# Kernel tuning notes

Measured on AMD Instinct MI355X. Metric: run time of the kernel, lower is better.

Reference implementation:

```python
import jax, jax.numpy as jnp
import numpy as np

NB_CLASSES = 100000
SZ_EMBED = 64
SZ_BATCH = 1024


def setup_inputs() -> dict:
    key = jax.random.key(0)
    k1, k2, k3 = jax.random.split(key, 3)
    xs = jax.random.normal(k1, (SZ_BATCH, SZ_EMBED), dtype=jnp.float32)
    ys = jax.random.randint(k2, (SZ_BATCH,), 0, NB_CLASSES, dtype=jnp.int64)
    # xavier_uniform for an Embedding(nb_classes, sz_embed)
    limit = float(np.sqrt(6.0 / (NB_CLASSES + SZ_EMBED)))
    proxies = jax.random.uniform(k3, (NB_CLASSES, SZ_EMBED), dtype=jnp.float32,
                                 minval=-limit, maxval=limit)
    return {"xs": xs, "ys": ys, "proxies": proxies}


def reference(xs, ys, proxies):
    # L2-normalize each proxy row (torch F.normalize; eps guard like torch's 1e-12).
    # Note: the original normalizes the positive proxy with dim=0 on a 1-D vector,
    # which is identical to per-row normalization.
    norms = jnp.linalg.norm(proxies, axis=1, keepdims=True)
    P = proxies / jnp.maximum(norms, 1e-12)                      # [C, D]

    # Squared euclidean distance matrix D[i, c] = ||x_i - P_c||^2 via GEMM
    x_sq = jnp.sum(xs * xs, axis=1, keepdims=True)               # [B, 1]
    p_sq = jnp.sum(P * P, axis=1)                                # [C]
    dist = jnp.maximum(x_sq + p_sq[None, :] - 2.0 * (xs @ P.T), 0.0)  # [B, C]

    logits = -dist                                               # [B, C]
    ys = ys.astype(jnp.int32)
    d_pos = jnp.take_along_axis(dist, ys[:, None], axis=1)[:, 0]  # [B]

    # log sum over negatives (c != y) of exp(-dist)
    neg_mask = jnp.arange(NB_CLASSES)[None, :] != ys[:, None]    # [B, C]
    neg_logits = jnp.where(neg_mask, logits, -jnp.inf)
    log_n = jax.nn.logsumexp(neg_logits, axis=1)                 # [B]

    # -log(p / n) = dist_pos + log(sum_neg exp(-dist))
    per_sample = d_pos + log_n
    return jnp.mean(per_sample)
```

## Files before the change

### kernel.cpp

```cpp
#include <hip/hip_runtime.h>
#include <math.h>

#define B 1024
#define C 100000
#define D 64
#define MT 128
#define TC 256
#define NCH 391
#define NPADROWS (NCH * TC)
#define CPAD (NPADROWS - C)
#define L2E 1.4426950408889634f
#define SCL2 (2.0f * L2E)

typedef __attribute__((ext_vector_type(8))) short short8;
typedef __attribute__((ext_vector_type(4))) float f32x4;

#define WS_PART 0
#define WS_CW2  ((size_t)NCH * B * 4)
#define WS_XBF  (WS_CW2 + B * 4)
#define WS_PBF  (WS_XBF + (size_t)B * D * 2)

#define GLB(p) ((const __attribute__((address_space(1))) void*)(p))
#define LDS(p) ((__attribute__((address_space(3))) void*)(p))

static __device__ __forceinline__ unsigned short f2bf(float f) {
    unsigned u = __float_as_uint(f);
    return (unsigned short)((u + 0x7fffu + ((u >> 16) & 1u)) >> 16);
}
static __device__ __forceinline__ float bf_round(float f) {
    return __uint_as_float(((unsigned)f2bf(f)) << 16);
}
static __device__ __forceinline__ float fexp2(float x) {
#if __has_builtin(__builtin_amdgcn_exp2f)
    return __builtin_amdgcn_exp2f(x);
#else
    return __expf(x * 0.6931471805599453f);
#endif
}

#define DPPF(x, ctrl) __uint_as_float((unsigned)__builtin_amdgcn_update_dpp( \
    0, (int)__float_as_uint(x), (ctrl), 0xF, 0xF, true))

__global__ __launch_bounds__(256) void proxynca_prep(
    const float* __restrict__ xs, const float* __restrict__ proxies,
    unsigned short* __restrict__ Xbf, unsigned short* __restrict__ Pbf,
    float* __restrict__ cw2, float* __restrict__ out)
{
    const int t = threadIdx.x;
    const int rl = t >> 4, f4 = t & 15;
    const int bb = blockIdx.x;
    if (bb == 0 && t == 0) out[0] = 0.f;
    if (bb < NPADROWS / 16) {
        int gr = bb * 16 + rl;
        float4 v = make_float4(0.f, 0.f, 0.f, 0.f);
        if (gr < C) v = *(const float4*)(proxies + (size_t)gr * D + f4 * 4);
        float ss = v.x*v.x + v.y*v.y + v.z*v.z + v.w*v.w;
        ss += __shfl_xor(ss, 1); ss += __shfl_xor(ss, 2);
        ss += __shfl_xor(ss, 4); ss += __shfl_xor(ss, 8);
        float rn = 1.0f / fmaxf(sqrtf(ss), 1e-12f);
        ushort4 w;
        w.x = f2bf(v.x * rn); w.y = f2bf(v.y * rn);
        w.z = f2bf(v.z * rn); w.w = f2bf(v.w * rn);
        *(ushort4*)(Pbf + (size_t)gr * D + f4 * 4) = w;
    } else {
        int row = (bb - NPADROWS / 16) * 16 + rl;
        float4 v = *(const float4*)(xs + (size_t)row * D + f4 * 4);
        float ss = v.x*v.x + v.y*v.y + v.z*v.z + v.w*v.w;
        ss += __shfl_xor(ss, 1); ss += __shfl_xor(ss, 2);
        ss += __shfl_xor(ss, 4); ss += __shfl_xor(ss, 8);
        ushort4 w;
        w.x = f2bf(v.x * SCL2); w.y = f2bf(v.y * SCL2);
        w.z = f2bf(v.z * SCL2); w.w = f2bf(v.w * SCL2);
        *(ushort4*)(Xbf + (size_t)row * D + f4 * 4) = w;
        if (f4 == 0) cw2[row] = -2.0f * sqrtf(ss) * L2E;
    }
}

__global__ __launch_bounds__(512, 4) void proxynca_main(
    const unsigned short* __restrict__ Xbf, const unsigned short* __restrict__ Pbf,
    const float* __restrict__ cw2v, float* __restrict__ partial)
{
    __shared__ __align__(16) unsigned short Ash[MT * 64];
    __shared__ __align__(16) unsigned short Bsh[TC * 64];
    __shared__ float rowsum[2][4][64];

    const int t = threadIdx.x;
    const int lane = t & 63;
    const int wv = t >> 6;
    const int row0 = blockIdx.x * MT;
    const int ct = blockIdx.y;

    const unsigned short* Asrc = Xbf + (size_t)row0 * D;
    const unsigned short* Bsrc = Pbf + (size_t)ct * TC * D;

    #pragma unroll
    for (int j = 0; j < 2; ++j) {
        int c = (j * 8 + wv) * 64 + lane;
        int row = c >> 3, q = c & 7;
        int sc = (row << 3) | (q ^ (row & 7));
        __builtin_amdgcn_global_load_lds(GLB(Asrc + sc * 8),
            LDS(Ash + (size_t)(j * 8 + wv) * 512), 16, 0, 0);
    }
    #pragma unroll
    for (int j = 0; j < 4; ++j) {
        int c = (j * 8 + wv) * 64 + lane;
        int row = c >> 3, q = c & 7;
        int sc = (row << 3) | (q ^ (row & 7));
        __builtin_amdgcn_global_load_lds(GLB(Bsrc + sc * 8),
            LDS(Bsh + (size_t)(j * 8 + wv) * 512), 16, 0, 0);
    }

    const int quad = lane >> 4, sixt = lane & 15;
    const int mg = wv >> 2, ng = wv & 3;

    f32x4 cwv[4];
    #pragma unroll
    for (int ms = 0; ms < 4; ++ms)
        cwv[ms] = *(const f32x4*)(cw2v + row0 + mg * 64 + ms * 16 + quad * 4);

    __syncthreads();

    short8 af[4][2];
    #pragma unroll
    for (int ms = 0; ms < 4; ++ms) {
        int rowL = mg * 64 + ms * 16 + sixt;
        int sw = rowL & 7;
        af[ms][0] = *(const short8*)(Ash + (size_t)(((rowL << 3) | (quad ^ sw)) * 8));
        af[ms][1] = *(const short8*)(Ash + (size_t)(((rowL << 3) | ((4 + quad) ^ sw)) * 8));
    }

    f32x4 s_vec[4];
    #pragma unroll
    for (int ms = 0; ms < 4; ++ms) s_vec[ms] = (f32x4){0.f, 0.f, 0.f, 0.f};

    #pragma unroll
    for (int ns = 0; ns < 4; ++ns) {
        int classL = ng * 64 + ns * 16 + sixt;
        int sw = classL & 7;
        short8 b0 = *(const short8*)(Bsh + (size_t)(((classL << 3) | (quad ^ sw)) * 8));
        short8 b1 = *(const short8*)(Bsh + (size_t)(((classL << 3) | ((4 + quad) ^ sw)) * 8));
        #pragma unroll
        for (int ms = 0; ms < 4; ++ms) {
            f32x4 acc = __builtin_amdgcn_mfma_f32_16x16x32_bf16(af[ms][0], b0, cwv[ms], 0, 0, 0);
            acc = __builtin_amdgcn_mfma_f32_16x16x32_bf16(af[ms][1], b1, acc, 0, 0, 0);
            f32x4 e;
            #pragma unroll
            for (int rg = 0; rg < 4; ++rg) e[rg] = fexp2(acc[rg]);
            s_vec[ms] += e;
        }
    }

    float v[16];
    #pragma unroll
    for (int ms = 0; ms < 4; ++ms)
        #pragma unroll
        for (int rg = 0; rg < 4; ++rg) v[ms * 4 + rg] = s_vec[ms][rg];

    {   bool b = (sixt & 8) != 0;
        #pragma unroll
        for (int j = 0; j < 8; ++j) {
            float k = b ? v[j + 8] : v[j];
            float s = b ? v[j] : v[j + 8];
            v[j] = k + DPPF(s, 0x140);
        }
    }
    {   bool b = (sixt & 4) != 0;
        #pragma unroll
        for (int j = 0; j < 4; ++j) {
            float k = b ? v[j + 4] : v[j];
            float s = b ? v[j] : v[j + 4];
            v[j] = k + DPPF(s, 0x141);
        }
    }
    {   bool b = (sixt & 2) != 0;
        #pragma unroll
        for (int j = 0; j < 2; ++j) {
            float k = b ? v[j + 2] : v[j];
            float s = b ? v[j] : v[j + 2];
            v[j] = k + DPPF(s, 0x4E);
        }
    }
    {   bool b = (sixt & 1) != 0;
        float k = b ? v[1] : v[0];
        float s = b ? v[0] : v[1];
        v[0] = k + DPPF(s, 0xB1);
    }

    int lrow = ((sixt >> 2) << 4) + (quad << 2) + (sixt & 3);
    rowsum[mg][ng][lrow] = v[0];
    __syncthreads();
    if (ng == 0) {
        float r = rowsum[mg][0][lane] + rowsum[mg][1][lane]
                + rowsum[mg][2][lane] + rowsum[mg][3][lane];
        partial[(size_t)ct * B + row0 + mg * 64 + lane] = r;
    }
}

__global__ __launch_bounds__(256) void proxynca_reduce(
    const float* __restrict__ xs, const int* __restrict__ ys,
    const float* __restrict__ proxies, const float* __restrict__ partial,
    float* __restrict__ out)
{
    __shared__ float acc4[4];
    const int lane = threadIdx.x & 63;
    const int w = threadIdx.x >> 6;
    const int row = blockIdx.x * 4 + w;

    float x = xs[(size_t)row * D + lane];
    int y = ys[row];
    float p = proxies[(size_t)y * D + lane];

    float xx = x * x, pp = p * p;
    #pragma unroll
    for (int off = 1; off < 64; off <<= 1) {
        xx += __shfl_xor(xx, off);
        pp += __shfl_xor(pp, off);
    }
    float nx = sqrtf(xx);
    float rn = 1.0f / fmaxf(sqrtf(pp), 1e-12f);
    float ph = p * rn;

    float xp = x * ph;
    float xpb = bf_round(x * SCL2) * bf_round(ph);
    #pragma unroll
    for (int off = 1; off < 64; off <<= 1) {
        xp  += __shfl_xor(xp, off);
        xpb += __shfl_xor(xpb, off);
    }

    float s = 0.f;
    for (int ct = lane; ct < NCH; ct += 64) s += partial[(size_t)ct * B + row];
    #pragma unroll
    for (int off = 1; off < 64; off <<= 1) s += __shfl_xor(s, off);

    if (lane == 0) {
        float cw2r = -2.0f * nx * L2E;
        float e_pos = fexp2(xpb + cw2r);
        float e_pad = fexp2(cw2r);
        float s_neg = s - e_pos - (float)CPAD * e_pad;
        acc4[w] = 2.0f * (nx - xp) + logf(s_neg);
    }
    __syncthreads();
    if (threadIdx.x == 0) {
        float v = acc4[0] + acc4[1] + acc4[2] + acc4[3];
        atomicAdd(out, v * (1.0f / (float)B));
    }
}

extern "C" void kernel_launch(void* const* d_in, const int* in_sizes, int n_in,
                              void* d_out, int out_size, void* d_ws, size_t ws_size,
                              hipStream_t stream)
{
    const float* xs      = (const float*)d_in[0];
    const int*   ys      = (const int*)d_in[1];
    const float* proxies = (const float*)d_in[2];
    char* ws = (char*)d_ws;
    float* partial = (float*)(ws + WS_PART);
    float* cw2     = (float*)(ws + WS_CW2);
    unsigned short* Xbf = (unsigned short*)(ws + WS_XBF);
    unsigned short* Pbf = (unsigned short*)(ws + WS_PBF);
    float* out = (float*)d_out;

    proxynca_prep<<<NPADROWS / 16 + B / 16, 256, 0, stream>>>(xs, proxies, Xbf, Pbf, cw2, out);
    dim3 gridA(B / MT, NCH);
    proxynca_main<<<gridA, 512, 0, stream>>>(Xbf, Pbf, cw2, partial);
    proxynca_reduce<<<B / 4, 256, 0, stream>>>(xs, ys, proxies, partial, out);
}
```

Before: 107.8 us.

## Fuse proxy/embedding normalization and bf16 conversion into the main GEMM kernel

Removes the separate prep kernel that normalized proxies and converted xs and proxies to bf16 in workspace. Each main-kernel block now loads raw fp32 rows, computes norms with DPP row reductions, converts to bf16 and writes the swizzled tiles straight into LDS, with the per-row constant also kept in LDS. This saves a kernel launch and the bf16 round trip through global memory. The cost is redundant work: every proxy tile is normalized 8 times (once per row block), each xs tile 391 times, and fp32 global reads double the bytes compared with bf16.

```diff
diff --git a/kernel.cpp b/kernel.cpp
--- a/kernel.cpp
+++ b/kernel.cpp
@@ -7,18 +7,12 @@
 #define MT 128
 #define TC 256
 #define NCH 391
-#define NPADROWS (NCH * TC)
-#define CPAD (NPADROWS - C)
+#define CPAD (NCH * TC - C)
 #define L2E 1.4426950408889634f
 #define SCL2 (2.0f * L2E)
 
 typedef __attribute__((ext_vector_type(8))) short short8;
 typedef __attribute__((ext_vector_type(4))) float f32x4;
-
-#define WS_PART 0
-#define WS_CW2  ((size_t)NCH * B * 4)
-#define WS_XBF  (WS_CW2 + B * 4)
-#define WS_PBF  (WS_XBF + (size_t)B * D * 2)
 
 #define GLB(p) ((const __attribute__((address_space(1))) void*)(p))
 #define LDS(p) ((__attribute__((address_space(3))) void*)(p))
@@ -41,47 +35,21 @@
 #define DPPF(x, ctrl) __uint_as_float((unsigned)__builtin_amdgcn_update_dpp( \
     0, (int)__float_as_uint(x), (ctrl), 0xF, 0xF, true))
 
-__global__ __launch_bounds__(256) void proxynca_prep(
+static __device__ __forceinline__ float row16_sum(float ss) {
+    ss += DPPF(ss, 0xB1);
+    ss += DPPF(ss, 0x4E);
+    ss += DPPF(ss, 0x141);
+    ss += DPPF(ss, 0x140);
+    return ss;
+}
+
+__global__ __launch_bounds__(512, 4) void proxynca_main(
     const float* __restrict__ xs, const float* __restrict__ proxies,
-    unsigned short* __restrict__ Xbf, unsigned short* __restrict__ Pbf,
-    float* __restrict__ cw2, float* __restrict__ out)
-{
-    const int t = threadIdx.x;
-    const int rl = t >> 4, f4 = t & 15;
-    const int bb = blockIdx.x;
-    if (bb == 0 && t == 0) out[0] = 0.f;
-    if (bb < NPADROWS / 16) {
-        int gr = bb * 16 + rl;
-        float4 v = make_float4(0.f, 0.f, 0.f, 0.f);
-        if (gr < C) v = *(const float4*)(proxies + (size_t)gr * D + f4 * 4);
-        float ss = v.x*v.x + v.y*v.y + v.z*v.z + v.w*v.w;
-        ss += __shfl_xor(ss, 1); ss += __shfl_xor(ss, 2);
-        ss += __shfl_xor(ss, 4); ss += __shfl_xor(ss, 8);
-        float rn = 1.0f / fmaxf(sqrtf(ss), 1e-12f);
-        ushort4 w;
-        w.x = f2bf(v.x * rn); w.y = f2bf(v.y * rn);
-        w.z = f2bf(v.z * rn); w.w = f2bf(v.w * rn);
-        *(ushort4*)(Pbf + (size_t)gr * D + f4 * 4) = w;
-    } else {
-        int row = (bb - NPADROWS / 16) * 16 + rl;
-        float4 v = *(const float4*)(xs + (size_t)row * D + f4 * 4);
-        float ss = v.x*v.x + v.y*v.y + v.z*v.z + v.w*v.w;
-        ss += __shfl_xor(ss, 1); ss += __shfl_xor(ss, 2);
-        ss += __shfl_xor(ss, 4); ss += __shfl_xor(ss, 8);
-        ushort4 w;
-        w.x = f2bf(v.x * SCL2); w.y = f2bf(v.y * SCL2);
-        w.z = f2bf(v.z * SCL2); w.w = f2bf(v.w * SCL2);
-        *(ushort4*)(Xbf + (size_t)row * D + f4 * 4) = w;
-        if (f4 == 0) cw2[row] = -2.0f * sqrtf(ss) * L2E;
-    }
-}
-
-__global__ __launch_bounds__(512, 4) void proxynca_main(
-    const unsigned short* __restrict__ Xbf, const unsigned short* __restrict__ Pbf,
-    const float* __restrict__ cw2v, float* __restrict__ partial)
+    float* __restrict__ partial, float* __restrict__ out)
 {
     __shared__ __align__(16) unsigned short Ash[MT * 64];
     __shared__ __align__(16) unsigned short Bsh[TC * 64];
+    __shared__ __align__(16) float crow[MT];
     __shared__ float rowsum[2][4][64];
 
     const int t = threadIdx.x;
@@ -89,26 +57,48 @@
     const int wv = t >> 6;
     const int row0 = blockIdx.x * MT;
     const int ct = blockIdx.y;
-
-    const unsigned short* Asrc = Xbf + (size_t)row0 * D;
-    const unsigned short* Bsrc = Pbf + (size_t)ct * TC * D;
-
-    #pragma unroll
-    for (int j = 0; j < 2; ++j) {
-        int c = (j * 8 + wv) * 64 + lane;
-        int row = c >> 3, q = c & 7;
-        int sc = (row << 3) | (q ^ (row & 7));
-        __builtin_amdgcn_global_load_lds(GLB(Asrc + sc * 8),
-            LDS(Ash + (size_t)(j * 8 + wv) * 512), 16, 0, 0);
-    }
-    #pragma unroll
-    for (int j = 0; j < 4; ++j) {
-        int c = (j * 8 + wv) * 64 + lane;
-        int row = c >> 3, q = c & 7;
-        int sc = (row << 3) | (q ^ (row & 7));
-        __builtin_amdgcn_global_load_lds(GLB(Bsrc + sc * 8),
-            LDS(Bsh + (size_t)(j * 8 + wv) * 512), 16, 0, 0);
-    }
+    const int prow = t >> 4;
+    const int f4 = t & 15;
+
+    if (blockIdx.x == 0 && ct == 0 && t == 0) out[0] = 0.f;
+
+    float4 pv[8];
+    #pragma unroll
+    for (int r = 0; r < 8; ++r) {
+        int gr = ct * TC + r * 32 + prow;
+        pv[r] = (gr < C) ? *(const float4*)(proxies + (size_t)gr * D + f4 * 4)
+                         : make_float4(0.f, 0.f, 0.f, 0.f);
+    }
+    float4 xv[4];
+    #pragma unroll
+    for (int r = 0; r < 4; ++r) {
+        int gr = row0 + r * 32 + prow;
+        xv[r] = *(const float4*)(xs + (size_t)gr * D + f4 * 4);
+    }
+
+    #pragma unroll
+    for (int r = 0; r < 8; ++r) {
+        float4 v = pv[r];
+        float ss = row16_sum(v.x*v.x + v.y*v.y + v.z*v.z + v.w*v.w);
+        float rn = 1.0f / fmaxf(sqrtf(ss), 1e-12f);
+        ushort4 w;
+        w.x = f2bf(v.x * rn); w.y = f2bf(v.y * rn);
+        w.z = f2bf(v.z * rn); w.w = f2bf(v.w * rn);
+        int row = r * 32 + prow;
+        *(ushort4*)(Bsh + (size_t)row * 64 + (((f4 >> 1) ^ (row & 7)) * 8) + (f4 & 1) * 4) = w;
+    }
+    #pragma unroll
+    for (int r = 0; r < 4; ++r) {
+        float4 v = xv[r];
+        float ss = row16_sum(v.x*v.x + v.y*v.y + v.z*v.z + v.w*v.w);
+        ushort4 w;
+        w.x = f2bf(v.x * SCL2); w.y = f2bf(v.y * SCL2);
+        w.z = f2bf(v.z * SCL2); w.w = f2bf(v.w * SCL2);
+        int row = r * 32 + prow;
+        *(ushort4*)(Ash + (size_t)row * 64 + (((f4 >> 1) ^ (row & 7)) * 8) + (f4 & 1) * 4) = w;
+        if (f4 == 0) crow[row] = -2.0f * sqrtf(ss) * L2E;
+    }
+    __syncthreads();
 
     const int quad = lane >> 4, sixt = lane & 15;
     const int mg = wv >> 2, ng = wv & 3;
@@ -116,9 +106,7 @@
     f32x4 cwv[4];
     #pragma unroll
     for (int ms = 0; ms < 4; ++ms)
-        cwv[ms] = *(const f32x4*)(cw2v + row0 + mg * 64 + ms * 16 + quad * 4);
-
-    __syncthreads();
+        cwv[ms] = *(const f32x4*)(crow + mg * 64 + ms * 16 + quad * 4);
 
     short8 af[4][2];
     #pragma unroll
@@ -254,15 +242,10 @@
     const float* xs      = (const float*)d_in[0];
     const int*   ys      = (const int*)d_in[1];
     const float* proxies = (const float*)d_in[2];
-    char* ws = (char*)d_ws;
-    float* partial = (float*)(ws + WS_PART);
-    float* cw2     = (float*)(ws + WS_CW2);
-    unsigned short* Xbf = (unsigned short*)(ws + WS_XBF);
-    unsigned short* Pbf = (unsigned short*)(ws + WS_PBF);
+    float* partial = (float*)d_ws;
     float* out = (float*)d_out;
 
-    proxynca_prep<<<NPADROWS / 16 + B / 16, 256, 0, stream>>>(xs, proxies, Xbf, Pbf, cw2, out);
     dim3 gridA(B / MT, NCH);
-    proxynca_main<<<gridA, 512, 0, stream>>>(Xbf, Pbf, cw2, partial);
+    proxynca_main<<<gridA, 512, 0, stream>>>(xs, proxies, partial, out);
     proxynca_reduce<<<B / 4, 256, 0, stream>>>(xs, ys, proxies, partial, out);
 }
```

Measured after the change: 126.1 us. +17.0%, slower.
